# Optimization experiments

Hardware: AMD Instinct MI355X
Metric: run time of the kernel (lower is better)

## Reference

```python
import jax, jax.numpy as jnp
import numpy as np

N_HEADS = 16
N_KV = 8
HEAD_DIM = 128
HID = 2048
GROUPS = N_HEADS // N_KV
THETA = 10000.0


def _rope_cos_sin(position_ids, dtype):
    # position_ids: [1, S] int
    inv_freq = 1.0 / (THETA ** (jnp.arange(0, HEAD_DIM, 2, dtype=jnp.float32) / HEAD_DIM))
    freqs = position_ids.astype(jnp.float32)[:, :, None] * inv_freq[None, None, :]  # [1,S,hd/2]
    emb = jnp.concatenate([freqs, freqs], axis=-1)  # [1,S,hd]
    return jnp.cos(emb).astype(dtype)[:, None, :, :], jnp.sin(emb).astype(dtype)[:, None, :, :]


def _rotate_half(x):
    x1, x2 = x[..., : HEAD_DIM // 2], x[..., HEAD_DIM // 2 :]
    return jnp.concatenate([-x2, x1], axis=-1)


def setup_inputs() -> dict:
    key = jax.random.key(0)
    ks = jax.random.split(key, 8)
    B, S = 2, 2048
    hidden_states = jax.random.normal(ks[0], (B, S, HID), jnp.float32)
    Wq = jax.random.normal(ks[1], (HID, N_HEADS * HEAD_DIM), jnp.float32) * 0.02
    Wk = jax.random.normal(ks[2], (HID, N_KV * HEAD_DIM), jnp.float32) * 0.02
    Wv = jax.random.normal(ks[3], (HID, N_KV * HEAD_DIM), jnp.float32) * 0.02
    Wo = jax.random.normal(ks[4], (HID, HID), jnp.float32) * 0.02
    gate = jnp.zeros((1, N_HEADS, 1, 1), jnp.float32)
    memory_in = jax.random.normal(ks[5], (B, N_KV, HEAD_DIM, HEAD_DIM), jnp.float32)
    norm_in = jax.random.uniform(ks[6], (B, N_KV, 1, HEAD_DIM), jnp.float32)
    position_ids = jnp.arange(S, dtype=jnp.int32)[None, :]
    return {"hidden_states": hidden_states, "Wq": Wq, "Wk": Wk, "Wv": Wv, "Wo": Wo,
            "gate": gate, "memory_in": memory_in, "norm_in": norm_in,
            "position_ids": position_ids}


def reference(hidden_states, Wq, Wk, Wv, Wo, gate, memory_in, norm_in, position_ids):
    B, S, _ = hidden_states.shape
    # projections -> [B, H, S, hd]
    q = jnp.einsum('bsh,ho->bso', hidden_states, Wq).reshape(B, S, N_HEADS, HEAD_DIM).transpose(0, 2, 1, 3)
    k = jnp.einsum('bsh,ho->bso', hidden_states, Wk).reshape(B, S, N_KV, HEAD_DIM).transpose(0, 2, 1, 3)
    v = jnp.einsum('bsh,ho->bso', hidden_states, Wv).reshape(B, S, N_KV, HEAD_DIM).transpose(0, 2, 1, 3)

    # ---- compressive memory retrieval (pre-RoPE q, as in original) ----
    sigma_q = jax.nn.elu(q) + 1.0  # [B, nH, S, hd]
    mem_tiled = jnp.tile(memory_in, (1, GROUPS, 1, 1))          # torch .repeat tiles
    norm_tiled = jnp.tile(norm_in, (1, GROUPS, 1, 1))            # [B, nH, 1, hd]
    memory_output = jnp.einsum('bhsd,bhde->bhse', sigma_q, mem_tiled)
    norm_bcast = jnp.einsum('bhsd,bhd->bhs', sigma_q, norm_tiled[:, :, 0, :])[..., None]
    memory_output = memory_output / norm_bcast

    # ---- memory update (pre-RoPE k, v) ----
    sigma_k = jax.nn.elu(k) + 1.0  # [B, nKV, S, hd]
    updated_memory = memory_in + jnp.einsum('bhsd,bhse->bhde', sigma_k, v)
    updated_norm = norm_in + jnp.sum(sigma_k, axis=2, keepdims=True)

    # ---- RoPE ----
    cos, sin = _rope_cos_sin(position_ids, q.dtype)
    q = q * cos + _rotate_half(q) * sin
    k = k * cos + _rotate_half(k) * sin

    # ---- repeat_kv (interleave, groups) ----
    k = jnp.repeat(k, GROUPS, axis=1)
    v = jnp.repeat(v, GROUPS, axis=1)

    # ---- causal SDPA ----
    scale = 1.0 / np.sqrt(HEAD_DIM)
    scores = jnp.einsum('bhqd,bhkd->bhqk', q, k) * scale
    causal = jnp.tril(jnp.ones((S, S), dtype=bool))
    scores = jnp.where(causal[None, None], scores, jnp.finfo(scores.dtype).min)
    probs = jax.nn.softmax(scores, axis=-1)
    attn = jnp.einsum('bhqk,bhkd->bhqd', probs, v)

    # ---- gated combination + output projection ----
    g = jax.nn.sigmoid(gate)
    combined = g * memory_output + (1.0 - g) * attn  # [B, nH, S, hd]
    combined = combined.transpose(0, 2, 1, 3).reshape(B, S, HID)
    final_output = jnp.einsum('bsh,ho->bso', combined, Wo)
    return final_output, updated_memory, updated_norm
```

## Files before the change

kernel.cpp:

```cpp
#include <hip/hip_runtime.h>

#define BATCH 2
#define SEQ   2048
#define HID   2048
#define NH    16
#define NKV   8
#define HD    128
#define M_ROWS (BATCH * SEQ)
#define QKV_N  4096

typedef __attribute__((ext_vector_type(8))) __bf16 bf16x8;
typedef __attribute__((ext_vector_type(4))) float  f32x4;

static __device__ __forceinline__ f32x4 mfma16(bf16x8 a, bf16x8 b, f32x4 c) {
    return __builtin_amdgcn_mfma_f32_16x16x32_bf16(a, b, c, 0, 0, 0);
}
static __device__ __forceinline__ float sigma_f(float x) {
    return x > 0.f ? x + 1.f : __expf(x);
}
static __device__ __forceinline__ void gload16(const __bf16* g, __bf16* l) {
    __builtin_amdgcn_global_load_lds(
        (const __attribute__((address_space(1))) void*)g,
        (__attribute__((address_space(3))) void*)l, 16, 0, 0);
}

#define OFF_QKV  0ull
#define OFF_SQ   67108864ull
#define OFF_QR   83886080ull
#define OFF_KR   100663296ull
#define OFF_VT   109051904ull
#define OFF_ND   117440512ull
#define OFF_CB   117702656ull
#define OFF_PART 134479872ull
#define OFF_BND  142868480ull
#define OFF_MAXP 143130624ull
#define OFF_NPART 143134720ull
#define NSPLIT 8

__global__ void f2b_k(const float* __restrict__ src, __bf16* __restrict__ dst)
{
    const size_t i = ((size_t)blockIdx.x * 256 + threadIdx.x) * 8;
    const float4 v0 = *reinterpret_cast<const float4*>(src + i);
    const float4 v1 = *reinterpret_cast<const float4*>(src + i + 4);
    bf16x8 t;
    t[0]=(__bf16)v0.x; t[1]=(__bf16)v0.y; t[2]=(__bf16)v0.z; t[3]=(__bf16)v0.w;
    t[4]=(__bf16)v1.x; t[5]=(__bf16)v1.y; t[6]=(__bf16)v1.z; t[7]=(__bf16)v1.w;
    *reinterpret_cast<bf16x8*>(dst + i) = t;
}

__global__ __launch_bounds__(256) void tr_k(const float* __restrict__ W,
                                            __bf16* __restrict__ Bt, int K, int N)
{
    __shared__ __bf16 T[64][72];
    const int k0 = blockIdx.x * 64, n0 = blockIdx.y * 64;
    const int t = threadIdx.x;
    #pragma unroll
    for (int i = 0; i < 4; ++i) {
        const int idx = t + i * 256;
        const int r = idx >> 4, c4 = (idx & 15) * 4;
        const float4 v = *reinterpret_cast<const float4*>(&W[(size_t)(k0 + r) * N + n0 + c4]);
        T[c4 + 0][r] = (__bf16)v.x; T[c4 + 1][r] = (__bf16)v.y;
        T[c4 + 2][r] = (__bf16)v.z; T[c4 + 3][r] = (__bf16)v.w;
    }
    __syncthreads();
    #pragma unroll
    for (int i = 0; i < 2; ++i) {
        const int idx = t + i * 256;
        const int rr = idx >> 3, cc = (idx & 7) * 8;
        *reinterpret_cast<bf16x8*>(&Bt[(size_t)(n0 + rr) * K + k0 + cc]) =
            *reinterpret_cast<bf16x8*>(&T[rr][cc]);
    }
}

__global__ __launch_bounds__(256) void gemm_bt(const __bf16* __restrict__ A,
                                               const __bf16* __restrict__ Bt,
                                               float* __restrict__ C,
                                               int N, int K)
{
    __shared__ __align__(16) __bf16 As[128 * 32];
    __shared__ __align__(16) __bf16 Bs[128 * 32];

    const int tid = threadIdx.x, wave = tid >> 6, lane = tid & 63;
    const int l15 = lane & 15, l4 = lane >> 4;
    const int m0 = blockIdx.x * 128, n0 = blockIdx.y * 128;
    const int wm = (wave & 1) * 64, wn = (wave >> 1) * 64;

    f32x4 acc[4][4] = {};

    const int srow = wave * 32 + (lane >> 2);
    const int scol = (lane & 3) * 8;
    const __bf16* Ab = A  + (size_t)(m0 + srow) * K + scol;
    const __bf16* Bb = Bt + (size_t)(n0 + srow) * K + scol;
    __bf16* AsB0 = &As[(wave * 32) * 32];
    __bf16* AsB1 = &As[(wave * 32 + 16) * 32];
    __bf16* BsB0 = &Bs[(wave * 32) * 32];
    __bf16* BsB1 = &Bs[(wave * 32 + 16) * 32];

    for (int kb = 0; kb < K; kb += 32) {
        gload16(Ab + kb,            AsB0);
        gload16(Ab + 16 * K + kb,   AsB1);
        gload16(Bb + kb,            BsB0);
        gload16(Bb + 16 * K + kb,   BsB1);
        __syncthreads();

        bf16x8 af[4], bfr[4];
        #pragma unroll
        for (int mt = 0; mt < 4; ++mt)
            af[mt] = *reinterpret_cast<bf16x8*>(&As[(wm + mt * 16 + l15) * 32 + l4 * 8]);
        #pragma unroll
        for (int nt = 0; nt < 4; ++nt)
            bfr[nt] = *reinterpret_cast<bf16x8*>(&Bs[(wn + nt * 16 + l15) * 32 + l4 * 8]);
        #pragma unroll
        for (int mt = 0; mt < 4; ++mt)
            #pragma unroll
            for (int nt = 0; nt < 4; ++nt)
                acc[mt][nt] = mfma16(af[mt], bfr[nt], acc[mt][nt]);
        __syncthreads();
    }

    #pragma unroll
    for (int mt = 0; mt < 4; ++mt)
        #pragma unroll
        for (int nt = 0; nt < 4; ++nt)
            #pragma unroll
            for (int r = 0; r < 4; ++r) {
                const int row = m0 + wm + mt * 16 + l4 * 4 + r;
                const int col = n0 + wn + nt * 16 + l15;
                C[(size_t)row * N + col] = acc[mt][nt][r];
            }
}

__global__ __launch_bounds__(256) void prep_k(const float* __restrict__ qkv,
                                              const float* __restrict__ norm_in,
                                              const int* __restrict__ pos_ids,
                                              __bf16* __restrict__ sq, __bf16* __restrict__ qr,
                                              __bf16* __restrict__ kr, __bf16* __restrict__ vt,
                                              float* __restrict__ nd, float* __restrict__ bnd,
                                              float* __restrict__ maxp)
{
    const int sc = blockIdx.x, kvh = blockIdx.y, b = blockIdx.z;
    const int s0 = sc * 32, t = threadIdx.x;
    const float scale = 0.08838834764831845f;
    const float s2 = scale * scale;
    const float NEG_LN_TH = -0.14391156831212787f;
    __shared__ float krn[32];

    {
        const int row = t >> 2;
        const int head = row >> 5, sl = row & 31;
        const int hq = kvh * 2 + head, nh = hq & 7;
        const int dq = (t & 3) * 16;
        const int pos = pos_ids[s0 + sl];
        const float* qp = qkv + (size_t)(b * SEQ + s0 + sl) * QKV_N + hq * 128;
        const float* np = norm_in + (b * NKV + nh) * 128;

        float x0[16], x1[16];
        #pragma unroll
        for (int i = 0; i < 16; i += 4) {
            *reinterpret_cast<float4*>(&x0[i]) = *reinterpret_cast<const float4*>(qp + dq + i);
            *reinterpret_cast<float4*>(&x1[i]) = *reinterpret_cast<const float4*>(qp + dq + 64 + i);
        }
        float nds = 0.f, qns = 0.f;
        bf16x8 sqv0[2], sqv1[2], qrv0[2], qrv1[2];
        #pragma unroll
        for (int i = 0; i < 16; ++i) {
            const int j = dq + i;
            float c, sn;
            __sincosf((float)pos * __expf((float)j * NEG_LN_TH), &sn, &c);
            qrv0[i >> 3][i & 7] = (__bf16)((x0[i] * c - x1[i] * sn) * scale);
            qrv1[i >> 3][i & 7] = (__bf16)((x1[i] * c + x0[i] * sn) * scale);
            const float sg0 = sigma_f(x0[i]), sg1 = sigma_f(x1[i]);
            sqv0[i >> 3][i & 7] = (__bf16)sg0;
            sqv1[i >> 3][i & 7] = (__bf16)sg1;
            nds += sg0 * np[j] + sg1 * np[j + 64];
            qns += (x0[i] * x0[i] + x1[i] * x1[i]) * s2;
        }
        __bf16* sqp = sq + ((size_t)(b * NH + hq) * SEQ + s0 + sl) * 128;
        __bf16* qrp = qr + ((size_t)(b * NH + hq) * SEQ + s0 + sl) * 128;
        *reinterpret_cast<bf16x8*>(sqp + dq)      = sqv0[0];
        *reinterpret_cast<bf16x8*>(sqp + dq + 8)  = sqv0[1];
        *reinterpret_cast<bf16x8*>(sqp + dq + 64) = sqv1[0];
        *reinterpret_cast<bf16x8*>(sqp + dq + 72) = sqv1[1];
        *reinterpret_cast<bf16x8*>(qrp + dq)      = qrv0[0];
        *reinterpret_cast<bf16x8*>(qrp + dq + 8)  = qrv0[1];
        *reinterpret_cast<bf16x8*>(qrp + dq + 64) = qrv1[0];
        *reinterpret_cast<bf16x8*>(qrp + dq + 72) = qrv1[1];

        nds += __shfl_xor(nds, 1); nds += __shfl_xor(nds, 2);
        qns += __shfl_xor(qns, 1); qns += __shfl_xor(qns, 2);
        if ((t & 3) == 0) {
            nd [(size_t)(b * NH + hq) * SEQ + s0 + sl] = nds;
            bnd[(size_t)(b * NH + hq) * SEQ + s0 + sl] = qns;
        }
    }

    if (t < 128) {
        const int sl = t >> 2;
        const int dq = (t & 3) * 16;
        const int pos = pos_ids[s0 + sl];
        const float* kp = qkv + (size_t)(b * SEQ + s0 + sl) * QKV_N + 2048 + kvh * 128;
        float x0[16], x1[16];
        #pragma unroll
        for (int i = 0; i < 16; i += 4) {
            *reinterpret_cast<float4*>(&x0[i]) = *reinterpret_cast<const float4*>(kp + dq + i);
            *reinterpret_cast<float4*>(&x1[i]) = *reinterpret_cast<const float4*>(kp + dq + 64 + i);
        }
        bf16x8 kv0[2], kv1[2];
        float kns = 0.f;
        #pragma unroll
        for (int i = 0; i < 16; ++i) {
            const int j = dq + i;
            float c, sn;
            __sincosf((float)pos * __expf((float)j * NEG_LN_TH), &sn, &c);
            kv0[i >> 3][i & 7] = (__bf16)(x0[i] * c - x1[i] * sn);
            kv1[i >> 3][i & 7] = (__bf16)(x1[i] * c + x0[i] * sn);
            kns += x0[i] * x0[i] + x1[i] * x1[i];
        }
        __bf16* krp = kr + ((size_t)(b * NKV + kvh) * SEQ + s0 + sl) * 128;
        *reinterpret_cast<bf16x8*>(krp + dq)      = kv0[0];
        *reinterpret_cast<bf16x8*>(krp + dq + 8)  = kv0[1];
        *reinterpret_cast<bf16x8*>(krp + dq + 64) = kv1[0];
        *reinterpret_cast<bf16x8*>(krp + dq + 72) = kv1[1];
        kns += __shfl_xor(kns, 1); kns += __shfl_xor(kns, 2);
        if ((t & 3) == 0) krn[sl] = kns;
    }

    __shared__ float vl[128][33];
    {
        const int sl = t >> 3, dch = (t & 7) * 16;
        const float* vp = qkv + (size_t)(b * SEQ + s0 + sl) * QKV_N + 3072 + kvh * 128 + dch;
        float xv[16];
        #pragma unroll
        for (int i = 0; i < 16; i += 4)
            *reinterpret_cast<float4*>(&xv[i]) = *reinterpret_cast<const float4*>(vp + i);
        #pragma unroll
        for (int i = 0; i < 16; ++i) vl[dch + i][sl] = xv[i];
    }
    __syncthreads();
    if (t == 0) {
        float mx = 0.f;
        #pragma unroll
        for (int i = 0; i < 32; ++i) mx = fmaxf(mx, krn[i]);
        maxp[((b * NKV + kvh) << 6) + sc] = mx;
    }
    {
        const int d = t >> 1, sh = (t & 1) * 16;
        bf16x8 o0, o1;
        #pragma unroll
        for (int j = 0; j < 8; ++j) o0[j] = (__bf16)vl[d][sh + j];
        #pragma unroll
        for (int j = 0; j < 8; ++j) o1[j] = (__bf16)vl[d][sh + 8 + j];
        __bf16* vp = vt + ((size_t)((b * NKV + kvh) * 128 + d)) * SEQ + s0 + sh;
        *reinterpret_cast<bf16x8*>(vp)     = o0;
        *reinterpret_cast<bf16x8*>(vp + 8) = o1;
    }
}

__global__ __launch_bounds__(256) void memout_k(const __bf16* __restrict__ sq,
                                                const float* __restrict__ mem_in,
                                                const float* __restrict__ nd,
                                                const float* __restrict__ gate,
                                                __bf16* __restrict__ cb)
{
    __shared__ __align__(16) __bf16 mt[128][136];
    const int tid = threadIdx.x;
    const int h = blockIdx.y, b = blockIdx.z;
    const int s0 = blockIdx.x * 64;

    const float* mem = mem_in + (size_t)(b * NKV + (h & 7)) * 16384;
    for (int i = tid; i < 16384; i += 256) {
        int dd = i >> 7, e = i & 127;
        mt[e][dd] = (__bf16)mem[i];
    }
    __syncthreads();

    const int wave = tid >> 6, lane = tid & 63, l15 = lane & 15, l4 = lane >> 4;
    f32x4 acc[8] = {};
    const __bf16* sqb = sq + ((size_t)(b * NH + h) * SEQ + s0 + wave * 16 + l15) * 128;
    #pragma unroll
    for (int kb = 0; kb < 4; ++kb) {
        bf16x8 a = *reinterpret_cast<const bf16x8*>(sqb + kb * 32 + l4 * 8);
        #pragma unroll
        for (int nc = 0; nc < 8; ++nc) {
            bf16x8 bb = *reinterpret_cast<bf16x8*>(&mt[nc * 16 + l15][kb * 32 + l4 * 8]);
            acc[nc] = mfma16(a, bb, acc[nc]);
        }
    }
    float g = 1.f / (1.f + __expf(-gate[h]));
    #pragma unroll
    for (int r = 0; r < 4; ++r) {
        int srow = s0 + wave * 16 + l4 * 4 + r;
        float scl = g / nd[(size_t)(b * NH + h) * SEQ + srow];
        __bf16* cbp = cb + (size_t)(b * SEQ + srow) * HID + h * 128;
        #pragma unroll
        for (int nc = 0; nc < 8; ++nc)
            cbp[nc * 16 + l15] = (__bf16)(acc[nc][r] * scl);
    }
}

__global__ __launch_bounds__(256) void memupd_k(const float* __restrict__ qkv,
                                                float* __restrict__ part,
                                                float* __restrict__ npart)
{
    const int sp = blockIdx.x, h = blockIdx.y, b = blockIdx.z;
    const int tid = threadIdx.x;
    const int tx = tid & 15, ty = tid >> 4;
    __shared__ __align__(16) float sk[8][128];
    __shared__ __align__(16) float sv[8][128];
    float acc[8][8] = {};
    float nacc = 0.f;

    const int s0 = sp * (SEQ / NSPLIT);
    for (int so = 0; so < SEQ / NSPLIT; so += 8) {
        for (int i = tid; i < 8 * 128; i += 256) {
            int rr = i >> 7, dd = i & 127;
            const float* rowp = qkv + (size_t)(b * SEQ + s0 + so + rr) * QKV_N;
            sk[rr][dd] = sigma_f(rowp[2048 + h * 128 + dd]);
            sv[rr][dd] = rowp[3072 + h * 128 + dd];
        }
        __syncthreads();
        if (tid < 128) {
            #pragma unroll
            for (int rr = 0; rr < 8; ++rr) nacc += sk[rr][tid];
        }
        #pragma unroll
        for (int rr = 0; rr < 8; ++rr) {
            float4 k0 = *reinterpret_cast<float4*>(&sk[rr][tx * 8]);
            float4 k1 = *reinterpret_cast<float4*>(&sk[rr][tx * 8 + 4]);
            float4 v0 = *reinterpret_cast<float4*>(&sv[rr][ty * 8]);
            float4 v1 = *reinterpret_cast<float4*>(&sv[rr][ty * 8 + 4]);
            float kreg[8] = {k0.x,k0.y,k0.z,k0.w,k1.x,k1.y,k1.z,k1.w};
            float vreg[8] = {v0.x,v0.y,v0.z,v0.w,v1.x,v1.y,v1.z,v1.w};
            #pragma unroll
            for (int i = 0; i < 8; ++i)
                #pragma unroll
                for (int j2 = 0; j2 < 8; ++j2)
                    acc[i][j2] += kreg[i] * vreg[j2];
        }
        __syncthreads();
    }
    float* pb = part + ((size_t)sp * (BATCH * NKV) + b * NKV + h) * 16384;
    #pragma unroll
    for (int i = 0; i < 8; ++i)
        #pragma unroll
        for (int j2 = 0; j2 < 8; ++j2)
            pb[(tx * 8 + i) * 128 + ty * 8 + j2] = acc[i][j2];
    if (tid < 128)
        npart[((size_t)sp * (BATCH * NKV) + b * NKV + h) * 128 + tid] = nacc;
}

__global__ void memred_k(const float* __restrict__ part, const float* __restrict__ mem_in,
                         float* __restrict__ out_mem)
{
    const size_t i = (size_t)blockIdx.x * 256 + threadIdx.x;
    float a = mem_in[i];
    #pragma unroll
    for (int sp = 0; sp < NSPLIT; ++sp) a += part[(size_t)sp * 262144 + i];
    out_mem[i] = a;
}

__global__ void normred_k(const float* __restrict__ npart, const float* __restrict__ norm_in,
                          float* __restrict__ out_norm)
{
    const int bh = blockIdx.x, d = threadIdx.x;
    float a = norm_in[bh * 128 + d];
    #pragma unroll
    for (int sp = 0; sp < NSPLIT; ++sp)
        a += npart[((size_t)sp * (BATCH * NKV) + bh) * 128 + d];
    out_norm[bh * 128 + d] = a;
}

__global__ __launch_bounds__(128) void attn_k(const __bf16* __restrict__ qr,
                                              const __bf16* __restrict__ kr,
                                              const __bf16* __restrict__ vt,
                                              const float* __restrict__ gate,
                                              const float* __restrict__ bnd,
                                              const float* __restrict__ maxp,
                                              __bf16* __restrict__ cb)
{
    __shared__ __align__(16) __bf16 Ks[64][136];
    __shared__ __align__(16) __bf16 Vs[128][72];
    __shared__ __align__(16) __bf16 plds[2][32][72];

    const int tid = threadIdx.x, wave = tid >> 6, lane = tid & 63;
    const int l15 = lane & 15, l4 = lane >> 4;
    const int h = blockIdx.y, b = blockIdx.z;
    const int kvh = h >> 1;

    const __bf16* kbase = kr + (size_t)(b * NKV + kvh) * SEQ * 128;
    const __bf16* vbase = vt + (size_t)(b * NKV + kvh) * 128 * SEQ;
    const float* bbase  = bnd + (size_t)(b * NH + h) * SEQ;

    const float g  = 1.f / (1.f + __expf(-gate[h]));
    const float gi = 1.f - g;
    float kn2 = 0.f;
    const float* mp = maxp + (b * NKV + kvh) * 64;
    #pragma unroll
    for (int i = 0; i < 64; i += 4) {
        const float4 v = *reinterpret_cast<const float4*>(mp + i);
        kn2 = fmaxf(kn2, fmaxf(fmaxf(v.x, v.y), fmaxf(v.z, v.w)));
    }
    const float knmax = sqrtf(kn2);

    bf16x8 ones;
    #pragma unroll
    for (int j = 0; j < 8; ++j) ones[j] = (__bf16)1.0f;

    const int ks_r = tid >> 4, ks_c = (tid & 15) * 8;
    const int vs_r = tid >> 3, vs_c = (tid & 7) * 8;

    #pragma unroll 1
    for (int tile = 0; tile < 2; ++tile) {
        const int q0 = (tile == 0 ? blockIdx.x : 31 - blockIdx.x) * 64;
        const int qw = q0 + wave * 32;

        bf16x8 af[2][4];
        float m_r[2][4];
        #pragma unroll
        for (int m = 0; m < 2; ++m) {
            const __bf16* qb = qr + ((size_t)(b * NH + h) * SEQ + qw + m * 16 + l15) * 128;
            #pragma unroll
            for (int kb = 0; kb < 4; ++kb)
                af[m][kb] = *reinterpret_cast<const bf16x8*>(qb + kb * 32 + l4 * 8);
            #pragma unroll
            for (int r = 0; r < 4; ++r)
                m_r[m][r] = sqrtf(bbase[qw + m * 16 + l4 * 4 + r]) * knmax + 1.0f;
        }

        f32x4 o0[8] = {}, o1[8] = {};
        f32x4 lc0 = {}, lc1 = {};

        #pragma unroll 1
        for (int kt = 0; kt < q0 + 64; kt += 64) {
            #pragma unroll
            for (int rr = 0; rr < 8; ++rr)
                *reinterpret_cast<bf16x8*>(&Ks[rr * 8 + ks_r][ks_c]) =
                    *reinterpret_cast<const bf16x8*>(kbase + (size_t)(kt + rr * 8 + ks_r) * 128 + ks_c);
            #pragma unroll
            for (int rr = 0; rr < 8; ++rr)
                *reinterpret_cast<bf16x8*>(&Vs[rr * 16 + vs_r][vs_c]) =
                    *reinterpret_cast<const bf16x8*>(vbase + (size_t)(rr * 16 + vs_r) * SEQ + kt + vs_c);
            __syncthreads();

            f32x4 s0[4] = {}, s1[4] = {};
            #pragma unroll
            for (int kb = 0; kb < 4; ++kb) {
                #pragma unroll
                for (int sub = 0; sub < 4; ++sub) {
                    bf16x8 bb = *reinterpret_cast<bf16x8*>(&Ks[sub * 16 + l15][kb * 32 + l4 * 8]);
                    s0[sub] = mfma16(af[0][kb], bb, s0[sub]);
                    s1[sub] = mfma16(af[1][kb], bb, s1[sub]);
                }
            }

            #pragma unroll
            for (int r = 0; r < 4; ++r) {
                const int q0r = qw + l4 * 4 + r;
                const int q1r = q0r + 16;
                #pragma unroll
                for (int sub = 0; sub < 4; ++sub) {
                    const int key = kt + sub * 16 + l15;
                    float p0 = __expf(s0[sub][r] - m_r[0][r]);
                    float p1 = __expf(s1[sub][r] - m_r[1][r]);
                    p0 = (key <= q0r) ? p0 : 0.f;
                    p1 = (key <= q1r) ? p1 : 0.f;
                    plds[wave][l4 * 4 + r][sub * 16 + l15]      = (__bf16)p0;
                    plds[wave][16 + l4 * 4 + r][sub * 16 + l15] = (__bf16)p1;
                }
            }

            bf16x8 a00 = *reinterpret_cast<bf16x8*>(&plds[wave][l15][l4 * 8]);
            bf16x8 a01 = *reinterpret_cast<bf16x8*>(&plds[wave][l15][32 + l4 * 8]);
            bf16x8 a10 = *reinterpret_cast<bf16x8*>(&plds[wave][16 + l15][l4 * 8]);
            bf16x8 a11 = *reinterpret_cast<bf16x8*>(&plds[wave][16 + l15][32 + l4 * 8]);
            lc0 = mfma16(a00, ones, lc0); lc0 = mfma16(a01, ones, lc0);
            lc1 = mfma16(a10, ones, lc1); lc1 = mfma16(a11, ones, lc1);
            #pragma unroll
            for (int nc = 0; nc < 8; ++nc) {
                bf16x8 b0 = *reinterpret_cast<bf16x8*>(&Vs[nc * 16 + l15][l4 * 8]);
                bf16x8 b1 = *reinterpret_cast<bf16x8*>(&Vs[nc * 16 + l15][32 + l4 * 8]);
                o0[nc] = mfma16(a00, b0, o0[nc]); o0[nc] = mfma16(a01, b1, o0[nc]);
                o1[nc] = mfma16(a10, b0, o1[nc]); o1[nc] = mfma16(a11, b1, o1[nc]);
            }
            __syncthreads();
        }

        #pragma unroll
        for (int r = 0; r < 4; ++r) {
            const int qrow = qw + l4 * 4 + r;
            const float i0 = gi / lc0[r];
            const float i1 = gi / lc1[r];
            __bf16* c0 = cb + (size_t)(b * SEQ + qrow) * HID + h * 128;
            __bf16* c1 = cb + (size_t)(b * SEQ + qrow + 16) * HID + h * 128;
            #pragma unroll
            for (int nc = 0; nc < 8; ++nc) {
                const int dd = nc * 16 + l15;
                c0[dd] = (__bf16)((float)c0[dd] + o0[nc][r] * i0);
                c1[dd] = (__bf16)((float)c1[dd] + o1[nc][r] * i1);
            }
        }
    }
}

extern "C" void kernel_launch(void* const* d_in, const int* in_sizes, int n_in,
                              void* d_out, int out_size, void* d_ws, size_t ws_size,
                              hipStream_t stream)
{
    const float* hidden  = (const float*)d_in[0];
    const float* Wq      = (const float*)d_in[1];
    const float* Wk      = (const float*)d_in[2];
    const float* Wv      = (const float*)d_in[3];
    const float* Wo      = (const float*)d_in[4];
    const float* gate    = (const float*)d_in[5];
    const float* mem_in  = (const float*)d_in[6];
    const float* norm_in = (const float*)d_in[7];
    const int*   pos     = (const int*)d_in[8];

    float* out_final = (float*)d_out;
    float* out_mem   = out_final + (size_t)BATCH * SEQ * HID;
    float* out_norm  = out_mem + (size_t)BATCH * NKV * 128 * 128;

    char* ws = (char*)d_ws;
    float*  qkv  = (float*)(ws + OFF_QKV);
    __bf16* sq   = (__bf16*)(ws + OFF_SQ);
    __bf16* qrb  = (__bf16*)(ws + OFF_QR);
    __bf16* krb  = (__bf16*)(ws + OFF_KR);
    __bf16* vtb  = (__bf16*)(ws + OFF_VT);
    float*  nd   = (float*)(ws + OFF_ND);
    __bf16* cb   = (__bf16*)(ws + OFF_CB);
    float*  part = (float*)(ws + OFF_PART);
    float*  bnd  = (float*)(ws + OFF_BND);
    float*  maxp = (float*)(ws + OFF_MAXP);
    float*  npart = (float*)(ws + OFF_NPART);
    __bf16* hb   = (__bf16*)(ws + OFF_SQ);
    __bf16* qkvT = (__bf16*)(ws + OFF_QR);
    __bf16* woT  = (__bf16*)(ws + OFF_PART);

    f2b_k<<<(M_ROWS * HID) / (256 * 8), 256, 0, stream>>>(hidden, hb);
    tr_k<<<dim3(HID / 64, 2048 / 64), 256, 0, stream>>>(Wq, qkvT, HID, 2048);
    tr_k<<<dim3(HID / 64, 1024 / 64), 256, 0, stream>>>(Wk, qkvT + (size_t)2048 * HID, HID, 1024);
    tr_k<<<dim3(HID / 64, 1024 / 64), 256, 0, stream>>>(Wv, qkvT + (size_t)3072 * HID, HID, 1024);

    gemm_bt<<<dim3(M_ROWS / 128, QKV_N / 128), 256, 0, stream>>>(hb, qkvT, qkv, QKV_N, HID);

    prep_k<<<dim3(SEQ / 32, NKV, BATCH), 256, 0, stream>>>(qkv, norm_in, pos, sq, qrb, krb, vtb,
                                                           nd, bnd, maxp);

    memout_k<<<dim3(SEQ / 64, NH, BATCH), 256, 0, stream>>>(sq, mem_in, nd, gate, cb);

    memupd_k<<<dim3(NSPLIT, NKV, BATCH), 256, 0, stream>>>(qkv, part, npart);
    memred_k<<<(BATCH * NKV * 128 * 128) / 256, 256, 0, stream>>>(part, mem_in, out_mem);
    normred_k<<<BATCH * NKV, 128, 0, stream>>>(npart, norm_in, out_norm);

    tr_k<<<dim3(HID / 64, HID / 64), 256, 0, stream>>>(Wo, woT, HID, HID);

    attn_k<<<dim3(16, NH, BATCH), 128, 0, stream>>>(qrb, krb, vtb, gate, bnd, maxp, cb);

    gemm_bt<<<dim3(M_ROWS / 128, HID / 128), 256, 0, stream>>>(cb, woT, out_final, HID, HID);
}
```

Before: 503.6 us.

## Split attention key range across four waves with async LDS loads and XCD remap

The attention kernel moves from 128 to 256 threads. Two wave pairs each take alternating 64-key sub-tiles of a 128-key chunk, and their partial outputs and row sums are combined through LDS at the end. K/V tiles are now loaded with global_load_lds using an XOR swizzle, replacing register staging and padded arrays. Block indices are remapped so that blocks sharing a KV head land on the same XCD for L2 reuse. This adds a cross-wave reduction and uses 80KB of LDS per block, which limits occupancy.

```diff
diff --git a/kernel.cpp b/kernel.cpp
--- a/kernel.cpp
+++ b/kernel.cpp
@@ -370,22 +370,32 @@
     out_norm[bh * 128 + d] = a;
 }
 
-__global__ __launch_bounds__(128) void attn_k(const __bf16* __restrict__ qr,
-                                              const __bf16* __restrict__ kr,
-                                              const __bf16* __restrict__ vt,
-                                              const float* __restrict__ gate,
-                                              const float* __restrict__ bnd,
-                                              const float* __restrict__ maxp,
-                                              __bf16* __restrict__ cb)
-{
-    __shared__ __align__(16) __bf16 Ks[64][136];
-    __shared__ __align__(16) __bf16 Vs[128][72];
-    __shared__ __align__(16) __bf16 plds[2][32][72];
+__global__ __launch_bounds__(256, 2) void attn_k(const __bf16* __restrict__ qr,
+                                                 const __bf16* __restrict__ kr,
+                                                 const __bf16* __restrict__ vt,
+                                                 const float* __restrict__ gate,
+                                                 const float* __restrict__ bnd,
+                                                 const float* __restrict__ maxp,
+                                                 __bf16* __restrict__ cb)
+{
+    __shared__ __align__(16) char smem[81920];
+    __bf16* Ks   = (__bf16*)smem;
+    __bf16* Vs   = (__bf16*)(smem + 32768);
+    __bf16* plds = (__bf16*)(smem + 65536);
+    float*  red  = (float*)smem;
+    float*  lred = (float*)(smem + 65536);
 
     const int tid = threadIdx.x, wave = tid >> 6, lane = tid & 63;
     const int l15 = lane & 15, l4 = lane >> 4;
-    const int h = blockIdx.y, b = blockIdx.z;
-    const int kvh = h >> 1;
+
+    const int n   = blockIdx.x + 16 * (blockIdx.y + 16 * blockIdx.z);
+    const int xcd = n & 7, i64 = n >> 3;
+    const int grp = xcd * 2 + (i64 >> 5);
+    const int within = i64 & 31;
+    const int b   = grp >> 3;
+    const int kvh = grp & 7;
+    const int h   = kvh * 2 + (within >> 4);
+    const int x   = within & 15;
 
     const __bf16* kbase = kr + (size_t)(b * NKV + kvh) * SEQ * 128;
     const __bf16* vbase = vt + (size_t)(b * NKV + kvh) * 128 * SEQ;
@@ -406,13 +416,20 @@
     #pragma unroll
     for (int j = 0; j < 8; ++j) ones[j] = (__bf16)1.0f;
 
-    const int ks_r = tid >> 4, ks_c = (tid & 15) * 8;
-    const int vs_r = tid >> 3, vs_c = (tid & 7) * 8;
+    const int srow = wave * 32 + (lane >> 4);
+    __bf16* ksd = Ks + wave * 4096;
+    __bf16* vsd = Vs + wave * 4096;
+
+    __bf16* pw = plds + wave * 2048;
+    const int ksub = wave >> 1;
+    const int wq   = wave & 1;
 
     #pragma unroll 1
     for (int tile = 0; tile < 2; ++tile) {
-        const int q0 = (tile == 0 ? blockIdx.x : 31 - blockIdx.x) * 64;
-        const int qw = q0 + wave * 32;
+        const int q0 = (tile == 0 ? x : 31 - x) * 64;
+        const int qw = q0 + wq * 32;
+        const int NT = (q0 >> 6) + 1;
+        const int NI = (NT + 1) >> 1;
 
         bf16x8 af[2][4];
         float m_r[2][4];
@@ -431,74 +448,110 @@
         f32x4 lc0 = {}, lc1 = {};
 
         #pragma unroll 1
-        for (int kt = 0; kt < q0 + 64; kt += 64) {
-            #pragma unroll
-            for (int rr = 0; rr < 8; ++rr)
-                *reinterpret_cast<bf16x8*>(&Ks[rr * 8 + ks_r][ks_c]) =
-                    *reinterpret_cast<const bf16x8*>(kbase + (size_t)(kt + rr * 8 + ks_r) * 128 + ks_c);
-            #pragma unroll
-            for (int rr = 0; rr < 8; ++rr)
-                *reinterpret_cast<bf16x8*>(&Vs[rr * 16 + vs_r][vs_c]) =
-                    *reinterpret_cast<const bf16x8*>(vbase + (size_t)(rr * 16 + vs_r) * SEQ + kt + vs_c);
+        for (int it = 0; it < NI; ++it) {
+            const int kt0 = it * 128;
+            #pragma unroll
+            for (int j = 0; j < 8; ++j) {
+                const int row = srow + j * 4;
+                const int ch  = (lane & 15) ^ (row & 7);
+                gload16(kbase + (size_t)(kt0 + row) * 128 + ch * 8, ksd + j * 512);
+                gload16(vbase + (size_t)row * SEQ + kt0 + ch * 8,   vsd + j * 512);
+            }
             __syncthreads();
 
-            f32x4 s0[4] = {}, s1[4] = {};
-            #pragma unroll
-            for (int kb = 0; kb < 4; ++kb) {
+            const int s = 2 * it + ksub;
+            if (s < NT) {
+                const int krow0 = ksub * 64;
+                f32x4 s0[4] = {}, s1[4] = {};
                 #pragma unroll
-                for (int sub = 0; sub < 4; ++sub) {
-                    bf16x8 bb = *reinterpret_cast<bf16x8*>(&Ks[sub * 16 + l15][kb * 32 + l4 * 8]);
-                    s0[sub] = mfma16(af[0][kb], bb, s0[sub]);
-                    s1[sub] = mfma16(af[1][kb], bb, s1[sub]);
+                for (int kb = 0; kb < 4; ++kb) {
+                    #pragma unroll
+                    for (int sub = 0; sub < 4; ++sub) {
+                        const int krow = krow0 + sub * 16 + l15;
+                        bf16x8 bb = *reinterpret_cast<const bf16x8*>(
+                            Ks + krow * 128 + (((kb * 4 + l4) ^ (krow & 7)) * 8));
+                        s0[sub] = mfma16(af[0][kb], bb, s0[sub]);
+                        s1[sub] = mfma16(af[1][kb], bb, s1[sub]);
+                    }
+                }
+                #pragma unroll
+                for (int r = 0; r < 4; ++r) {
+                    const int q0r = qw + l4 * 4 + r;
+                    const int q1r = q0r + 16;
+                    const int p0r = l4 * 4 + r, p1r = p0r + 16;
+                    #pragma unroll
+                    for (int sub = 0; sub < 4; ++sub) {
+                        const int key = s * 64 + sub * 16 + l15;
+                        float p0 = __expf(s0[sub][r] - m_r[0][r]);
+                        float p1 = __expf(s1[sub][r] - m_r[1][r]);
+                        p0 = (key <= q0r) ? p0 : 0.f;
+                        p1 = (key <= q1r) ? p1 : 0.f;
+                        const int cc = (sub * 16 + l15) >> 3, cl = l15 & 7;
+                        pw[p0r * 64 + ((cc ^ (p0r & 7)) * 8) + cl] = (__bf16)p0;
+                        pw[p1r * 64 + ((cc ^ (p1r & 7)) * 8) + cl] = (__bf16)p1;
+                    }
+                }
+                const int pr1 = 16 + l15;
+                bf16x8 a00 = *reinterpret_cast<bf16x8*>(pw + l15 * 64 + ((l4 ^ (l15 & 7)) * 8));
+                bf16x8 a01 = *reinterpret_cast<bf16x8*>(pw + l15 * 64 + (((4 + l4) ^ (l15 & 7)) * 8));
+                bf16x8 a10 = *reinterpret_cast<bf16x8*>(pw + pr1 * 64 + ((l4 ^ (pr1 & 7)) * 8));
+                bf16x8 a11 = *reinterpret_cast<bf16x8*>(pw + pr1 * 64 + (((4 + l4) ^ (pr1 & 7)) * 8));
+                lc0 = mfma16(a00, ones, lc0); lc0 = mfma16(a01, ones, lc0);
+                lc1 = mfma16(a10, ones, lc1); lc1 = mfma16(a11, ones, lc1);
+                #pragma unroll
+                for (int nc = 0; nc < 8; ++nc) {
+                    const int vrow = nc * 16 + l15;
+                    bf16x8 b0 = *reinterpret_cast<bf16x8*>(
+                        Vs + vrow * 128 + (((ksub * 8 + l4) ^ (vrow & 7)) * 8));
+                    bf16x8 b1 = *reinterpret_cast<bf16x8*>(
+                        Vs + vrow * 128 + (((ksub * 8 + 4 + l4) ^ (vrow & 7)) * 8));
+                    o0[nc] = mfma16(a00, b0, o0[nc]); o0[nc] = mfma16(a01, b1, o0[nc]);
+                    o1[nc] = mfma16(a10, b0, o1[nc]); o1[nc] = mfma16(a11, b1, o1[nc]);
                 }
             }
-
-            #pragma unroll
-            for (int r = 0; r < 4; ++r) {
-                const int q0r = qw + l4 * 4 + r;
-                const int q1r = q0r + 16;
+            __syncthreads();
+        }
+
+        if (wave >= 2) {
+            float* rb = red + (wave - 2) * 4224;
+            #pragma unroll
+            for (int nc = 0; nc < 8; ++nc)
                 #pragma unroll
-                for (int sub = 0; sub < 4; ++sub) {
-                    const int key = kt + sub * 16 + l15;
-                    float p0 = __expf(s0[sub][r] - m_r[0][r]);
-                    float p1 = __expf(s1[sub][r] - m_r[1][r]);
-                    p0 = (key <= q0r) ? p0 : 0.f;
-                    p1 = (key <= q1r) ? p1 : 0.f;
-                    plds[wave][l4 * 4 + r][sub * 16 + l15]      = (__bf16)p0;
-                    plds[wave][16 + l4 * 4 + r][sub * 16 + l15] = (__bf16)p1;
+                for (int r = 0; r < 4; ++r) {
+                    rb[(l4 * 4 + r) * 132 + nc * 16 + l15]        = o0[nc][r];
+                    rb[(16 + l4 * 4 + r) * 132 + nc * 16 + l15]   = o1[nc][r];
+                }
+            if (l15 == 0) {
+                float* lb = lred + (wave - 2) * 32;
+                #pragma unroll
+                for (int r = 0; r < 4; ++r) {
+                    lb[l4 * 4 + r]      = lc0[r];
+                    lb[16 + l4 * 4 + r] = lc1[r];
                 }
             }
-
-            bf16x8 a00 = *reinterpret_cast<bf16x8*>(&plds[wave][l15][l4 * 8]);
-            bf16x8 a01 = *reinterpret_cast<bf16x8*>(&plds[wave][l15][32 + l4 * 8]);
-            bf16x8 a10 = *reinterpret_cast<bf16x8*>(&plds[wave][16 + l15][l4 * 8]);
-            bf16x8 a11 = *reinterpret_cast<bf16x8*>(&plds[wave][16 + l15][32 + l4 * 8]);
-            lc0 = mfma16(a00, ones, lc0); lc0 = mfma16(a01, ones, lc0);
-            lc1 = mfma16(a10, ones, lc1); lc1 = mfma16(a11, ones, lc1);
-            #pragma unroll
-            for (int nc = 0; nc < 8; ++nc) {
-                bf16x8 b0 = *reinterpret_cast<bf16x8*>(&Vs[nc * 16 + l15][l4 * 8]);
-                bf16x8 b1 = *reinterpret_cast<bf16x8*>(&Vs[nc * 16 + l15][32 + l4 * 8]);
-                o0[nc] = mfma16(a00, b0, o0[nc]); o0[nc] = mfma16(a01, b1, o0[nc]);
-                o1[nc] = mfma16(a10, b0, o1[nc]); o1[nc] = mfma16(a11, b1, o1[nc]);
+        }
+        __syncthreads();
+        if (wave < 2) {
+            float* rb = red + wave * 4224;
+            const float* lb = lred + wave * 32;
+            #pragma unroll
+            for (int r = 0; r < 4; ++r) {
+                const int qrow = qw + l4 * 4 + r;
+                const float i0 = gi / (lc0[r] + lb[l4 * 4 + r]);
+                const float i1 = gi / (lc1[r] + lb[16 + l4 * 4 + r]);
+                __bf16* c0 = cb + (size_t)(b * SEQ + qrow) * HID + h * 128;
+                __bf16* c1 = cb + (size_t)(b * SEQ + qrow + 16) * HID + h * 128;
+                #pragma unroll
+                for (int nc = 0; nc < 8; ++nc) {
+                    const int dd = nc * 16 + l15;
+                    const float v0 = o0[nc][r] + rb[(l4 * 4 + r) * 132 + dd];
+                    const float v1 = o1[nc][r] + rb[(16 + l4 * 4 + r) * 132 + dd];
+                    c0[dd] = (__bf16)((float)c0[dd] + v0 * i0);
+                    c1[dd] = (__bf16)((float)c1[dd] + v1 * i1);
+                }
             }
-            __syncthreads();
-        }
-
-        #pragma unroll
-        for (int r = 0; r < 4; ++r) {
-            const int qrow = qw + l4 * 4 + r;
-            const float i0 = gi / lc0[r];
-            const float i1 = gi / lc1[r];
-            __bf16* c0 = cb + (size_t)(b * SEQ + qrow) * HID + h * 128;
-            __bf16* c1 = cb + (size_t)(b * SEQ + qrow + 16) * HID + h * 128;
-            #pragma unroll
-            for (int nc = 0; nc < 8; ++nc) {
-                const int dd = nc * 16 + l15;
-                c0[dd] = (__bf16)((float)c0[dd] + o0[nc][r] * i0);
-                c1[dd] = (__bf16)((float)c1[dd] + o1[nc][r] * i1);
-            }
-        }
+        }
+        __syncthreads();
     }
 }
 
@@ -554,7 +607,7 @@
 
     tr_k<<<dim3(HID / 64, HID / 64), 256, 0, stream>>>(Wo, woT, HID, HID);
 
-    attn_k<<<dim3(16, NH, BATCH), 128, 0, stream>>>(qrb, krb, vtb, gate, bnd, maxp, cb);
+    attn_k<<<dim3(16, NH, BATCH), 256, 0, stream>>>(qrb, krb, vtb, gate, bnd, maxp, cb);
 
     gemm_bt<<<dim3(M_ROWS / 128, HID / 128), 256, 0, stream>>>(cb, woT, out_final, HID, HID);
 }
```

Measured after the change: 475.0 us. -5.7%, faster.
